# Optimization experiments

Hardware: AMD Instinct MI355X
Metric: run time of the kernel (lower is better)

## Reference

```python
import jax, jax.numpy as jnp
import numpy as np

B, L, HID, H = 4, 1024, 1024, 16
D = HID // H  # 64

def setup_inputs() -> dict:
    key = jax.random.key(0)
    ks = jax.random.split(key, 9)
    s = 0.02
    return {
        'query_states': jax.random.normal(ks[0], (B, L, HID), jnp.float32),
        'key_states':   jax.random.normal(ks[1], (B, L, HID), jnp.float32),
        'value_states': jax.random.normal(ks[2], (B, L, HID), jnp.float32),
        'Wq': jax.random.normal(ks[3], (HID, HID), jnp.float32) * s,
        'bq': jnp.zeros((HID,), jnp.float32),
        'Wk': jax.random.normal(ks[4], (HID, HID), jnp.float32) * s,
        'bk': jnp.zeros((HID,), jnp.float32),
        'Wv': jax.random.normal(ks[5], (HID, HID), jnp.float32) * s,
        'bv': jnp.zeros((HID,), jnp.float32),
        'Wo': jax.random.normal(ks[6], (HID, HID), jnp.float32) * s,
        'bo': jnp.zeros((HID,), jnp.float32),
        'rel_pos_enc': jax.random.normal(ks[7], (2 * L - 1, D), jnp.float32),
    }

def _split_heads(x):
    # [B,L,HID] -> [B,H,L,D]
    return x.reshape(B, L, H, D).transpose(0, 2, 1, 3)

def reference(query_states, key_states, value_states, Wq, bq, Wk, bk, Wv, bv, Wo, bo, rel_pos_enc):
    q = _split_heads(query_states @ Wq + bq)  # [B,H,L,D]
    k = _split_heads(key_states @ Wk + bk)
    v = _split_heads(value_states @ Wv + bv)
    scores = jnp.einsum('bhld,bhrd->bhlr', q, k)
    # relative position bias
    pos = jnp.arange(L)
    distance = pos[:, None] - pos[None, :] + L - 1          # [L,L] in [0, 2L-2]
    pos_emb = rel_pos_enc[distance]                          # [L,L,D]
    scores = scores + jnp.einsum('bhld,lrd->bhlr', q, pos_emb)
    scores = scores / jnp.sqrt(jnp.asarray(D, scores.dtype))
    probs = jax.nn.softmax(scores, axis=-1)                  # dropout p=0 (eval)
    ctx = jnp.einsum('bhlr,bhrd->bhld', probs, v)
    ctx = ctx.transpose(0, 2, 1, 3).reshape(B, L, HID)
    out = ctx @ Wo + bo
    return (out, probs)
```

## Files before the change

kernel.cpp:

```cpp
#include <hip/hip_runtime.h>

typedef __bf16 bf16_t;
typedef bf16_t bf16x8 __attribute__((ext_vector_type(8)));
typedef bf16_t bf16x4 __attribute__((ext_vector_type(4)));
typedef float f32x16 __attribute__((ext_vector_type(16)));
typedef float f32x4v __attribute__((ext_vector_type(4)));
typedef unsigned int u32;

#define DEVI __device__ __forceinline__

DEVI f32x16 zero16() {
  f32x16 z;
#pragma unroll
  for (int i = 0; i < 16; ++i) z[i] = 0.0f;
  return z;
}

DEVI void gload16(const bf16_t* g, const unsigned short* l) {
  __builtin_amdgcn_global_load_lds(
      (const __attribute__((address_space(1))) u32*)g,
      (__attribute__((address_space(3))) u32*)l, 16, 0, 0);
}

union U16B { bf16x8 v; uint4 u; unsigned short s[8]; };
union U4B  { bf16_t h[4]; uint2 u; };

__global__ __launch_bounds__(256) void prep_kernel(
    const float* __restrict__ W0, const float* __restrict__ W1,
    const float* __restrict__ W2, const float* __restrict__ W3,
    bf16_t* __restrict__ T0, bf16_t* __restrict__ T1,
    bf16_t* __restrict__ T2, bf16_t* __restrict__ T3,
    const float* __restrict__ xq, const float* __restrict__ xk,
    const float* __restrict__ xv, const float* __restrict__ relE,
    bf16_t* __restrict__ xqb, bf16_t* __restrict__ xkb,
    bf16_t* __restrict__ xvb, bf16_t* __restrict__ Eb) {
  __shared__ float T[64][65];
  const int bid = blockIdx.x;
  const int tid = threadIdx.x;
  if (bid < 1024) {
    const int sel = bid >> 8;
    const float* W = sel == 0 ? W0 : sel == 1 ? W1 : sel == 2 ? W2 : W3;
    bf16_t* Wt = sel == 0 ? T0 : sel == 1 ? T1 : sel == 2 ? T2 : T3;
    const int bx = bid & 255;
    const int tx = bx & 15, ty = bx >> 4;
    const int k0 = ty * 64, n0 = tx * 64;
    {
      const int r = tid >> 4, c4 = (tid & 15) * 4;
#pragma unroll
      for (int rr = 0; rr < 64; rr += 16) {
        float4 v = *reinterpret_cast<const float4*>(&W[(size_t)(k0 + r + rr) * 1024 + n0 + c4]);
        T[r + rr][c4 + 0] = v.x; T[r + rr][c4 + 1] = v.y;
        T[r + rr][c4 + 2] = v.z; T[r + rr][c4 + 3] = v.w;
      }
    }
    __syncthreads();
    {
      const int r = tid >> 3, c8 = (tid & 7) * 8;
#pragma unroll
      for (int rr = 0; rr < 64; rr += 32) {
        U16B p;
#pragma unroll
        for (int i = 0; i < 8; ++i) p.v[i] = (bf16_t)T[c8 + i][r + rr];
        *reinterpret_cast<uint4*>(&Wt[(size_t)(n0 + r + rr) * 1024 + k0 + c8]) = p.u;
      }
    }
  } else {
    for (int u = (bid - 1024) * 256 + tid; u < 3178496; u += 2048 * 256) {
      if (u < 3145728) {
        const int which = u >> 20;
        const float* src = which == 0 ? xq : which == 1 ? xk : xv;
        bf16_t* dst = which == 0 ? xqb : which == 1 ? xkb : xvb;
        const size_t off = (size_t)(u & 1048575) * 4;
        float4 v = *reinterpret_cast<const float4*>(&src[off]);
        U4B p;
        p.h[0] = (bf16_t)v.x; p.h[1] = (bf16_t)v.y; p.h[2] = (bf16_t)v.z; p.h[3] = (bf16_t)v.w;
        *reinterpret_cast<uint2*>(&dst[off]) = p.u;
      } else {
        const int q = u - 3145728;
        U4B p;
        if (q < 32752) {
          float4 v = *reinterpret_cast<const float4*>(&relE[(size_t)q * 4]);
          p.h[0] = (bf16_t)v.x; p.h[1] = (bf16_t)v.y; p.h[2] = (bf16_t)v.z; p.h[3] = (bf16_t)v.w;
        } else {
          p.h[0] = p.h[1] = p.h[2] = p.h[3] = (bf16_t)0.0f;
        }
        *reinterpret_cast<uint2*>(&Eb[(size_t)q * 4]) = p.u;
      }
    }
  }
}

#define ROWMAP(reg) (((reg) & 3) + 8 * ((reg) >> 2) + 4 * hi)
template <int MODE>
__global__ __launch_bounds__(256) void gemm_kernel(
    const bf16_t* __restrict__ A0, const bf16_t* __restrict__ A1,
    const bf16_t* __restrict__ A2, const bf16_t* __restrict__ W0,
    const bf16_t* __restrict__ W1, const bf16_t* __restrict__ W2,
    const float* __restrict__ b0, const float* __restrict__ b1,
    const float* __restrict__ b2, void* __restrict__ O0,
    void* __restrict__ O1, void* __restrict__ O2) {
  __shared__ __align__(16) unsigned short As[128][64];
  __shared__ __align__(16) unsigned short Bs[128][64];
  const int f = blockIdx.x;
  int op, r;
  const bf16_t *Ap, *Wt;
  const float* bias;
  void* Out;
  if constexpr (MODE == 0) {
    const int fp = (f & 7) * 96 + (f >> 3);
    op = fp >> 8; r = fp & 255;
    Ap = op == 0 ? A0 : op == 1 ? A1 : A2;
    Wt = op == 0 ? W0 : op == 1 ? W1 : W2;
    bias = op == 0 ? b0 : op == 1 ? b1 : b2;
    Out = op == 0 ? O0 : op == 1 ? O1 : O2;
  } else {
    const int fp = (f & 7) * 32 + (f >> 3);
    op = 0; r = fp;
    Ap = A0; Wt = W0; bias = b0; Out = O0;
  }
  const int m0 = (r >> 3) * 128, n0 = (r & 7) * 128;
  const int tid = threadIdx.x;
  const int lane = tid & 63, wave = tid >> 6;
  const int hi = lane >> 5, ln = lane & 31;
  const int wr = wave >> 1, wc = wave & 1;
  const int srow = lane >> 3, scol = lane & 7;

  f32x16 acc[2][2];
  acc[0][0] = zero16(); acc[0][1] = zero16();
  acc[1][0] = zero16(); acc[1][1] = zero16();

  for (int k0 = 0; k0 < 1024; k0 += 64) {
#pragma unroll
    for (int j = 0; j < 4; ++j) {
      const int rowbase = wave * 32 + j * 8;
      const int row = rowbase + srow;
      const int gc = scol ^ (row & 7);
      gload16(&Ap[(size_t)(m0 + row) * 1024 + k0 + gc * 8], &As[rowbase][0]);
      gload16(&Wt[(size_t)(n0 + row) * 1024 + k0 + gc * 8], &Bs[rowbase][0]);
    }
    __syncthreads();
#pragma unroll
    for (int kk = 0; kk < 4; ++kk) {
      const int ch = kk * 2 + hi;
      const int ar0 = wr * 64 + ln, ar1 = ar0 + 32;
      const int br0 = wc * 64 + ln, br1 = br0 + 32;
      bf16x8 a0 = *reinterpret_cast<const bf16x8*>(&As[ar0][(ch ^ (ar0 & 7)) * 8]);
      bf16x8 a1 = *reinterpret_cast<const bf16x8*>(&As[ar1][(ch ^ (ar1 & 7)) * 8]);
      bf16x8 bb0 = *reinterpret_cast<const bf16x8*>(&Bs[br0][(ch ^ (br0 & 7)) * 8]);
      bf16x8 bb1 = *reinterpret_cast<const bf16x8*>(&Bs[br1][(ch ^ (br1 & 7)) * 8]);
      acc[0][0] = __builtin_amdgcn_mfma_f32_32x32x16_bf16(a0, bb0, acc[0][0], 0, 0, 0);
      acc[0][1] = __builtin_amdgcn_mfma_f32_32x32x16_bf16(a0, bb1, acc[0][1], 0, 0, 0);
      acc[1][0] = __builtin_amdgcn_mfma_f32_32x32x16_bf16(a1, bb0, acc[1][0], 0, 0, 0);
      acc[1][1] = __builtin_amdgcn_mfma_f32_32x32x16_bf16(a1, bb1, acc[1][1], 0, 0, 0);
    }
    __syncthreads();
  }
#pragma unroll
  for (int cb = 0; cb < 2; ++cb) {
    const int nc = n0 + wc * 64 + cb * 32 + ln;
    const float bv = bias[nc];
    if constexpr (MODE == 2) {
#pragma unroll
      for (int rb = 0; rb < 2; ++rb)
#pragma unroll
        for (int reg = 0; reg < 16; ++reg) {
          const int mr = m0 + wr * 64 + rb * 32 + ROWMAP(reg);
          ((float*)Out)[(size_t)mr * 1024 + nc] = acc[rb][cb][reg] + bv;
        }
    } else {
      const int h = nc >> 6, d = nc & 63;
      if (op < 2) {
#pragma unroll
        for (int rb = 0; rb < 2; ++rb)
#pragma unroll
          for (int reg = 0; reg < 16; ++reg) {
            const int mr = m0 + wr * 64 + rb * 32 + ROWMAP(reg);
            const int b = mr >> 10, l = mr & 1023;
            ((bf16_t*)Out)[(((size_t)(b * 16 + h)) * 1024 + l) * 64 + d] =
                (bf16_t)(acc[rb][cb][reg] + bv);
          }
      } else {
#pragma unroll
        for (int rb = 0; rb < 2; ++rb)
#pragma unroll
          for (int g = 0; g < 4; ++g) {
            const int l4 = m0 + wr * 64 + rb * 32 + g * 8 + 4 * hi;
            const int b = l4 >> 10, ll = l4 & 1023;
            U4B p;
#pragma unroll
            for (int j = 0; j < 4; ++j) p.h[j] = (bf16_t)(acc[rb][cb][g * 4 + j] + bv);
            *reinterpret_cast<uint2*>(
                &((bf16_t*)Out)[(((size_t)(b * 16 + h)) * 64 + d) * 1024 + ll]) = p.u;
          }
      }
    }
  }
}

__global__ __launch_bounds__(512, 4) void attn_kernel(
    const bf16_t* __restrict__ q, const bf16_t* __restrict__ k,
    const bf16_t* __restrict__ vt, const bf16_t* __restrict__ E,
    float* __restrict__ probs, bf16_t* __restrict__ ctx) {
  __shared__ __align__(16) unsigned short Pbuf[8][32][128];
  __shared__ float rstat[32][9];
  const int f = blockIdx.x;
  const int fp = (f & 7) * 256 + (f >> 3);
  const int bh = fp >> 5;
  const int l0 = (fp & 31) * 32;
  const int tid = threadIdx.x;
  const int lane = tid & 63, wave = tid >> 6;
  const int hi = lane >> 5, ln = lane & 31;
  const bf16_t* qb = q + (size_t)bh * 1024 * 64;
  const bf16_t* kb = k + (size_t)bh * 1024 * 64;
  const bf16_t* vb = vt + (size_t)bh * 64 * 1024;
  const int rbase = wave * 128;
  const int b0 = l0 - rbase + 992;

  bf16x8 qf[4];
#pragma unroll
  for (int kk = 0; kk < 4; ++kk)
    qf[kk] = *reinterpret_cast<const bf16x8*>(&qb[(size_t)(l0 + ln) * 64 + kk * 16 + hi * 8]);

  f32x16 tpre = zero16();
  __builtin_amdgcn_s_setprio(1);
#pragma unroll
  for (int kk = 0; kk < 4; ++kk) {
    bf16x8 e = *reinterpret_cast<const bf16x8*>(
        &E[(size_t)(b0 + 32 + ln) * 64 + kk * 16 + hi * 8]);
    tpre = __builtin_amdgcn_mfma_f32_32x32x16_bf16(qf[kk], e, tpre, 0, 0, 0);
  }
  __builtin_amdgcn_s_setprio(0);

#pragma unroll
  for (int t = 0; t < 4; ++t) {
    const int r0 = rbase + t * 32;
    f32x16 acc = zero16();
    f32x16 tcur = zero16();
    __builtin_amdgcn_s_setprio(1);
#pragma unroll
    for (int kk = 0; kk < 4; ++kk) {
      bf16x8 kf = *reinterpret_cast<const bf16x8*>(
          &kb[(size_t)(r0 + ln) * 64 + kk * 16 + hi * 8]);
      acc = __builtin_amdgcn_mfma_f32_32x32x16_bf16(qf[kk], kf, acc, 0, 0, 0);
      bf16x8 e = *reinterpret_cast<const bf16x8*>(
          &E[(size_t)(b0 - 32 * t + ln) * 64 + kk * 16 + hi * 8]);
      tcur = __builtin_amdgcn_mfma_f32_32x32x16_bf16(qf[kk], e, tcur, 0, 0, 0);
    }
    __builtin_amdgcn_s_setprio(0);
#pragma unroll
    for (int reg = 0; reg < 16; ++reg) {
      const int i = ROWMAP(reg);
      const int w = i - ln + 31;
      const int src = (w & 31) + (hi << 5);
      acc[reg] += __shfl((ln >= i) ? tcur[reg] : tpre[reg], src, 64);
    }
    const int col = t * 32 + ln;
#pragma unroll
    for (int reg = 0; reg < 16; ++reg) {
      const int i = ROWMAP(reg);
      union { bf16_t h; unsigned short u; } cv;
      cv.h = (bf16_t)exp2f(acc[reg] * 0.1803368801f);
      Pbuf[wave][i][((col >> 3) ^ (i & 7)) * 8 + (col & 7)] = cv.u;
    }
    tpre = tcur;
  }

  {
    float s = 0.0f;
#pragma unroll
    for (int g = 0; g < 8; ++g) {
      const int cg = hi * 8 + g;
      bf16x8 pv = *reinterpret_cast<const bf16x8*>(
          &Pbuf[wave][ln][((cg ^ (ln & 7))) * 8]);
#pragma unroll
      for (int e = 0; e < 8; ++e) s += (float)pv[e];
    }
    s += __shfl_xor(s, 32, 64);
    if (hi == 0) rstat[ln][wave] = s;
  }

  f32x16 pv0 = zero16(), pv1 = zero16();
  __builtin_amdgcn_s_setprio(1);
#pragma unroll
  for (int kk = 0; kk < 8; ++kk) {
    const int ch = kk * 2 + hi;
    bf16x8 pa = *reinterpret_cast<const bf16x8*>(&Pbuf[wave][ln][(ch ^ (ln & 7)) * 8]);
    bf16x8 v0 = *reinterpret_cast<const bf16x8*>(
        &vb[(size_t)ln * 1024 + rbase + kk * 16 + hi * 8]);
    bf16x8 v1 = *reinterpret_cast<const bf16x8*>(
        &vb[(size_t)(32 + ln) * 1024 + rbase + kk * 16 + hi * 8]);
    pv0 = __builtin_amdgcn_mfma_f32_32x32x16_bf16(pa, v0, pv0, 0, 0, 0);
    pv1 = __builtin_amdgcn_mfma_f32_32x32x16_bf16(pa, v1, pv1, 0, 0, 0);
  }
  __builtin_amdgcn_s_setprio(0);

  __syncthreads();

  float inv;
  {
    float s = 0.0f;
#pragma unroll
    for (int w = 0; w < 8; ++w) s += rstat[ln][w];
    inv = 1.0f / s;
  }

  float* pb = probs + ((size_t)bh * 1024 + l0) * 1024;
#pragma unroll
  for (int it = 0; it < 16; ++it) {
    const int r = it * 2 + hi;
    const float invr = __shfl(inv, r, 64);
    const int g = ln >> 1;
    bf16x4 pv = *reinterpret_cast<const bf16x4*>(
        &Pbuf[wave][r][(g ^ (r & 7)) * 8 + (ln & 1) * 4]);
    f32x4v o;
    o[0] = (float)pv[0] * invr; o[1] = (float)pv[1] * invr;
    o[2] = (float)pv[2] * invr; o[3] = (float)pv[3] * invr;
    __builtin_nontemporal_store(
        o, reinterpret_cast<f32x4v*>(&pb[(size_t)r * 1024 + rbase + ln * 4]));
  }

  float* cred = reinterpret_cast<float*>(&Pbuf[0][0][0]);
  if (wave < 4) {
#pragma unroll
    for (int reg = 0; reg < 16; ++reg) {
      const int i = ROWMAP(reg);
      cred[((size_t)wave * 32 + i) * 64 + ln] = pv0[reg];
      cred[((size_t)wave * 32 + i) * 64 + 32 + ln] = pv1[reg];
    }
  }
  __syncthreads();
  if (wave >= 4) {
    const int s = wave - 4;
#pragma unroll
    for (int reg = 0; reg < 16; ++reg) {
      const int i = ROWMAP(reg);
      cred[((size_t)s * 32 + i) * 64 + ln] += pv0[reg];
      cred[((size_t)s * 32 + i) * 64 + 32 + ln] += pv1[reg];
    }
  }
  __syncthreads();
  {
    const int i = tid >> 4, d0 = (tid & 15) * 4;
    float4 a = *reinterpret_cast<const float4*>(&cred[(size_t)(0 * 32 + i) * 64 + d0]);
#pragma unroll
    for (int s = 1; s < 4; ++s) {
      float4 b = *reinterpret_cast<const float4*>(&cred[(size_t)(s * 32 + i) * 64 + d0]);
      a.x += b.x; a.y += b.y; a.z += b.z; a.w += b.w;
    }
    const float invr = __shfl(inv, i, 64);
    U4B o;
    o.h[0] = (bf16_t)(a.x * invr); o.h[1] = (bf16_t)(a.y * invr);
    o.h[2] = (bf16_t)(a.z * invr); o.h[3] = (bf16_t)(a.w * invr);
    const int b = bh >> 4, h = bh & 15;
    *reinterpret_cast<uint2*>(&ctx[((((size_t)b * 1024) + l0 + i) * 16 + h) * 64 + d0]) = o.u;
  }
}

extern "C" void kernel_launch(void* const* d_in, const int* in_sizes, int n_in,
                              void* d_out, int out_size, void* d_ws, size_t ws_size,
                              hipStream_t stream) {
  const float* xq = (const float*)d_in[0];
  const float* xk = (const float*)d_in[1];
  const float* xv = (const float*)d_in[2];
  const float* Wq = (const float*)d_in[3];
  const float* bq = (const float*)d_in[4];
  const float* Wk = (const float*)d_in[5];
  const float* bk = (const float*)d_in[6];
  const float* Wv = (const float*)d_in[7];
  const float* bv = (const float*)d_in[8];
  const float* Wo = (const float*)d_in[9];
  const float* bo = (const float*)d_in[10];
  const float* relE = (const float*)d_in[11];

  char* ws = (char*)d_ws;
  const size_t MB2 = 1u << 21;
  bf16_t* WtQ = (bf16_t*)(ws + 0 * MB2);
  bf16_t* WtK = (bf16_t*)(ws + 1 * MB2);
  bf16_t* WtV = (bf16_t*)(ws + 2 * MB2);
  bf16_t* WtO = (bf16_t*)(ws + 3 * MB2);
  bf16_t* Eb  = (bf16_t*)(ws + 4 * MB2);
  bf16_t* qb  = (bf16_t*)(ws + 4 * MB2 + (1u << 19));
  bf16_t* kb  = qb + (size_t)4 * 16 * 1024 * 64;
  bf16_t* vtb = kb + (size_t)4 * 16 * 1024 * 64;
  bf16_t* ctxb = vtb + (size_t)4 * 16 * 1024 * 64;

  float* outp = (float*)d_out;
  float* probs = outp + (size_t)4 * 1024 * 1024;
  bf16_t* xqb = (bf16_t*)probs;
  bf16_t* xkb = xqb + (size_t)4 * 1024 * 1024;
  bf16_t* xvb = xkb + (size_t)4 * 1024 * 1024;

  prep_kernel<<<3072, 256, 0, stream>>>(Wq, Wk, Wv, Wo, WtQ, WtK, WtV, WtO,
                                        xq, xk, xv, relE, xqb, xkb, xvb, Eb);
  gemm_kernel<0><<<768, 256, 0, stream>>>(xqb, xkb, xvb, WtQ, WtK, WtV,
                                          bq, bk, bv, qb, kb, vtb);
  attn_kernel<<<2048, 512, 0, stream>>>(qb, kb, vtb, Eb, probs, ctxb);
  gemm_kernel<2><<<256, 256, 0, stream>>>(ctxb, nullptr, nullptr, WtO, nullptr, nullptr,
                                          bo, nullptr, nullptr, outp, nullptr, nullptr);
}
```

Baseline: 200.3 us.

## Compute softmax row sums via MFMA, widen probs stores, simplify ctx reduction

Row sums of the exponentiated scores are now produced by an extra MFMA against a vector of ones inside the PV loop, replacing the separate LDS read-and-add pass. exp2f is replaced by the hardware exp2 builtin. The probs write-out now uses 8-element LDS reads and two 16-byte stores per lane. The two-stage cross-wave ctx reduction is replaced by every wave writing its partial into its own Pbuf slice, followed by one 8-way sum, which removes a barrier. The costs are an extra MFMA per step and a sum taken from bf16 values at MFMA precision, with a different rounding order.

```diff
diff --git a/kernel.cpp b/kernel.cpp
--- a/kernel.cpp
+++ b/kernel.cpp
@@ -14,6 +14,14 @@
 #pragma unroll
   for (int i = 0; i < 16; ++i) z[i] = 0.0f;
   return z;
+}
+
+DEVI float fast_exp2(float x) {
+#if __has_builtin(__builtin_amdgcn_exp2f)
+  return __builtin_amdgcn_exp2f(x);
+#else
+  return exp2f(x);
+#endif
 }
 
 DEVI void gload16(const bf16_t* g, const unsigned short* l) {
@@ -259,27 +267,16 @@
     for (int reg = 0; reg < 16; ++reg) {
       const int i = ROWMAP(reg);
       union { bf16_t h; unsigned short u; } cv;
-      cv.h = (bf16_t)exp2f(acc[reg] * 0.1803368801f);
+      cv.h = (bf16_t)fast_exp2(acc[reg] * 0.1803368801f);
       Pbuf[wave][i][((col >> 3) ^ (i & 7)) * 8 + (col & 7)] = cv.u;
     }
     tpre = tcur;
   }
 
-  {
-    float s = 0.0f;
-#pragma unroll
-    for (int g = 0; g < 8; ++g) {
-      const int cg = hi * 8 + g;
-      bf16x8 pv = *reinterpret_cast<const bf16x8*>(
-          &Pbuf[wave][ln][((cg ^ (ln & 7))) * 8]);
-#pragma unroll
-      for (int e = 0; e < 8; ++e) s += (float)pv[e];
-    }
-    s += __shfl_xor(s, 32, 64);
-    if (hi == 0) rstat[ln][wave] = s;
-  }
-
-  f32x16 pv0 = zero16(), pv1 = zero16();
+  bf16x8 ones;
+#pragma unroll
+  for (int e = 0; e < 8; ++e) ones[e] = (bf16_t)1.0f;
+  f32x16 pv0 = zero16(), pv1 = zero16(), pvs = zero16();
   __builtin_amdgcn_s_setprio(1);
 #pragma unroll
   for (int kk = 0; kk < 8; ++kk) {
@@ -291,9 +288,16 @@
         &vb[(size_t)(32 + ln) * 1024 + rbase + kk * 16 + hi * 8]);
     pv0 = __builtin_amdgcn_mfma_f32_32x32x16_bf16(pa, v0, pv0, 0, 0, 0);
     pv1 = __builtin_amdgcn_mfma_f32_32x32x16_bf16(pa, v1, pv1, 0, 0, 0);
+    pvs = __builtin_amdgcn_mfma_f32_32x32x16_bf16(pa, ones, pvs, 0, 0, 0);
   }
   __builtin_amdgcn_s_setprio(0);
 
+  {
+    float s = 0.0f;
+#pragma unroll
+    for (int reg = 0; reg < 16; ++reg) s = ((ln & 15) == reg) ? pvs[reg] : s;
+    if (ln < 16) rstat[ROWMAP(ln)][wave] = s;
+  }
   __syncthreads();
 
   float inv;
@@ -305,46 +309,42 @@
   }
 
   float* pb = probs + ((size_t)bh * 1024 + l0) * 1024;
-#pragma unroll
-  for (int it = 0; it < 16; ++it) {
-    const int r = it * 2 + hi;
-    const float invr = __shfl(inv, r, 64);
-    const int g = ln >> 1;
-    bf16x4 pv = *reinterpret_cast<const bf16x4*>(
-        &Pbuf[wave][r][(g ^ (r & 7)) * 8 + (ln & 1) * 4]);
-    f32x4v o;
-    o[0] = (float)pv[0] * invr; o[1] = (float)pv[1] * invr;
-    o[2] = (float)pv[2] * invr; o[3] = (float)pv[3] * invr;
-    __builtin_nontemporal_store(
-        o, reinterpret_cast<f32x4v*>(&pb[(size_t)r * 1024 + rbase + ln * 4]));
-  }
-
-  float* cred = reinterpret_cast<float*>(&Pbuf[0][0][0]);
-  if (wave < 4) {
-#pragma unroll
-    for (int reg = 0; reg < 16; ++reg) {
-      const int i = ROWMAP(reg);
-      cred[((size_t)wave * 32 + i) * 64 + ln] = pv0[reg];
-      cred[((size_t)wave * 32 + i) * 64 + 32 + ln] = pv1[reg];
-    }
-  }
-  __syncthreads();
-  if (wave >= 4) {
-    const int s = wave - 4;
-#pragma unroll
-    for (int reg = 0; reg < 16; ++reg) {
-      const int i = ROWMAP(reg);
-      cred[((size_t)s * 32 + i) * 64 + ln] += pv0[reg];
-      cred[((size_t)s * 32 + i) * 64 + 32 + ln] += pv1[reg];
-    }
+  {
+    const int rsub = lane >> 4;
+    const int pg = lane & 15;
+#pragma unroll
+    for (int it = 0; it < 8; ++it) {
+      const int r = it * 4 + rsub;
+      const float invr = __shfl(inv, r, 64);
+      bf16x8 pv = *reinterpret_cast<const bf16x8*>(
+          &Pbuf[wave][r][(pg ^ (r & 7)) * 8]);
+      f32x4v o0, o1;
+      o0[0] = (float)pv[0] * invr; o0[1] = (float)pv[1] * invr;
+      o0[2] = (float)pv[2] * invr; o0[3] = (float)pv[3] * invr;
+      o1[0] = (float)pv[4] * invr; o1[1] = (float)pv[5] * invr;
+      o1[2] = (float)pv[6] * invr; o1[3] = (float)pv[7] * invr;
+      float* dst = &pb[(size_t)r * 1024 + rbase + pg * 8];
+      __builtin_nontemporal_store(o0, reinterpret_cast<f32x4v*>(dst));
+      __builtin_nontemporal_store(o1, reinterpret_cast<f32x4v*>(dst + 4));
+    }
+  }
+
+  float* credw = reinterpret_cast<float*>(&Pbuf[wave][0][0]);
+#pragma unroll
+  for (int reg = 0; reg < 16; ++reg) {
+    const int i = ROWMAP(reg);
+    credw[(size_t)i * 64 + ln] = pv0[reg];
+    credw[(size_t)i * 64 + 32 + ln] = pv1[reg];
   }
   __syncthreads();
   {
     const int i = tid >> 4, d0 = (tid & 15) * 4;
-    float4 a = *reinterpret_cast<const float4*>(&cred[(size_t)(0 * 32 + i) * 64 + d0]);
-#pragma unroll
-    for (int s = 1; s < 4; ++s) {
-      float4 b = *reinterpret_cast<const float4*>(&cred[(size_t)(s * 32 + i) * 64 + d0]);
+    const float* cred = reinterpret_cast<const float*>(&Pbuf[0][0][0]);
+    float4 a = *reinterpret_cast<const float4*>(&cred[(size_t)i * 64 + d0]);
+#pragma unroll
+    for (int s = 1; s < 8; ++s) {
+      float4 b = *reinterpret_cast<const float4*>(
+          &cred[(size_t)s * 2048 + (size_t)i * 64 + d0]);
       a.x += b.x; a.y += b.y; a.z += b.z; a.w += b.w;
     }
     const float invr = __shfl(inv, i, 64);
```

Result: slower. 237.5 us (+18.6%).

## Use 256x256 double-buffered tiles for the fused QKV projection GEMM

Applied to the files above, without the earlier changes.

Splits the templated GEMM into a dedicated QKV kernel and an output-projection kernel. The QKV kernel now uses 512-thread blocks over 256x256 tiles with two LDS buffers, prefetching the next K-tile via async global-to-LDS loads while computing on the current one (vmcnt-based waits instead of full syncs). This targets load latency and operand reuse at the cost of larger LDS use (128KB per block), fewer blocks (192 on a machine with many CUs), and more register pressure.

```diff
diff --git a/kernel.cpp b/kernel.cpp
--- a/kernel.cpp
+++ b/kernel.cpp
@@ -91,33 +91,128 @@
 }
 
 #define ROWMAP(reg) (((reg) & 3) + 8 * ((reg) >> 2) + 4 * hi)
-template <int MODE>
-__global__ __launch_bounds__(256) void gemm_kernel(
+
+__global__ __launch_bounds__(512, 2) void gemm_qkv_kernel(
     const bf16_t* __restrict__ A0, const bf16_t* __restrict__ A1,
     const bf16_t* __restrict__ A2, const bf16_t* __restrict__ W0,
     const bf16_t* __restrict__ W1, const bf16_t* __restrict__ W2,
     const float* __restrict__ b0, const float* __restrict__ b1,
-    const float* __restrict__ b2, void* __restrict__ O0,
-    void* __restrict__ O1, void* __restrict__ O2) {
+    const float* __restrict__ b2, bf16_t* __restrict__ O0,
+    bf16_t* __restrict__ O1, bf16_t* __restrict__ O2) {
+  __shared__ __align__(16) unsigned short As[2][256][64];
+  __shared__ __align__(16) unsigned short Bs[2][256][64];
+  const int f = blockIdx.x;
+  const int fp = (f & 7) * 24 + (f >> 3);
+  const int op = fp >> 6;
+  const int r = fp & 63;
+  const bf16_t* Ap = op == 0 ? A0 : op == 1 ? A1 : A2;
+  const bf16_t* Wt = op == 0 ? W0 : op == 1 ? W1 : W2;
+  const float* bias = op == 0 ? b0 : op == 1 ? b1 : b2;
+  bf16_t* Out = op == 0 ? O0 : op == 1 ? O1 : O2;
+  const int m0 = (r >> 2) * 256, n0 = (r & 3) * 256;
+  const int tid = threadIdx.x;
+  const int lane = tid & 63, wave = tid >> 6;
+  const int hi = lane >> 5, ln = lane & 31;
+  const int wr = wave >> 2, wc = wave & 3;
+  const int srow = lane >> 3, scol = lane & 7;
+
+  f32x16 acc[4][2];
+#pragma unroll
+  for (int rt = 0; rt < 4; ++rt) { acc[rt][0] = zero16(); acc[rt][1] = zero16(); }
+
+#define STAGE(kt, buf)                                                              \
+  {                                                                                 \
+    _Pragma("unroll")                                                               \
+    for (int j = 0; j < 4; ++j) {                                                   \
+      const int rowbase = wave * 32 + j * 8;                                        \
+      const int row = rowbase + srow;                                               \
+      const int gc = scol ^ (row & 7);                                              \
+      gload16(&Ap[(size_t)(m0 + row) * 1024 + (kt) * 64 + gc * 8],                  \
+              &As[buf][rowbase][0]);                                                \
+      gload16(&Wt[(size_t)(n0 + row) * 1024 + (kt) * 64 + gc * 8],                  \
+              &Bs[buf][rowbase][0]);                                                \
+    }                                                                               \
+  }
+
+  STAGE(0, 0);
+  STAGE(1, 1);
+
+  for (int kt = 0; kt < 16; ++kt) {
+    const int cur = kt & 1;
+    if (kt < 15) {
+      asm volatile("s_waitcnt vmcnt(8)" ::: "memory");
+    } else {
+      asm volatile("s_waitcnt vmcnt(0)" ::: "memory");
+    }
+    __builtin_amdgcn_s_barrier();
+    __builtin_amdgcn_sched_barrier(0);
+#pragma unroll
+    for (int kk = 0; kk < 4; ++kk) {
+      const int ch = kk * 2 + hi;
+      bf16x8 a[4], b[2];
+#pragma unroll
+      for (int rt = 0; rt < 4; ++rt) {
+        const int ar = wr * 128 + rt * 32 + ln;
+        a[rt] = *reinterpret_cast<const bf16x8*>(&As[cur][ar][(ch ^ (ar & 7)) * 8]);
+      }
+#pragma unroll
+      for (int ct = 0; ct < 2; ++ct) {
+        const int br = wc * 64 + ct * 32 + ln;
+        b[ct] = *reinterpret_cast<const bf16x8*>(&Bs[cur][br][(ch ^ (br & 7)) * 8]);
+      }
+#pragma unroll
+      for (int rt = 0; rt < 4; ++rt)
+#pragma unroll
+        for (int ct = 0; ct < 2; ++ct)
+          acc[rt][ct] = __builtin_amdgcn_mfma_f32_32x32x16_bf16(a[rt], b[ct], acc[rt][ct], 0, 0, 0);
+    }
+    __builtin_amdgcn_sched_barrier(0);
+    __builtin_amdgcn_s_barrier();
+    __builtin_amdgcn_sched_barrier(0);
+    if (kt + 2 < 16) STAGE(kt + 2, cur);
+  }
+#undef STAGE
+
+#pragma unroll
+  for (int ct = 0; ct < 2; ++ct) {
+    const int nc = n0 + wc * 64 + ct * 32 + ln;
+    const float bv = bias[nc];
+    const int h = nc >> 6, d = nc & 63;
+    if (op < 2) {
+#pragma unroll
+      for (int rt = 0; rt < 4; ++rt)
+#pragma unroll
+        for (int reg = 0; reg < 16; ++reg) {
+          const int mr = m0 + wr * 128 + rt * 32 + ROWMAP(reg);
+          const int b = mr >> 10, l = mr & 1023;
+          Out[(((size_t)(b * 16 + h)) * 1024 + l) * 64 + d] =
+              (bf16_t)(acc[rt][ct][reg] + bv);
+        }
+    } else {
+#pragma unroll
+      for (int rt = 0; rt < 4; ++rt)
+#pragma unroll
+        for (int g = 0; g < 4; ++g) {
+          const int l4 = m0 + wr * 128 + rt * 32 + g * 8 + 4 * hi;
+          const int b = l4 >> 10, ll = l4 & 1023;
+          U4B p;
+#pragma unroll
+          for (int j = 0; j < 4; ++j) p.h[j] = (bf16_t)(acc[rt][ct][g * 4 + j] + bv);
+          *reinterpret_cast<uint2*>(
+              &Out[(((size_t)(b * 16 + h)) * 64 + d) * 1024 + ll]) = p.u;
+        }
+    }
+  }
+}
+
+__global__ __launch_bounds__(256) void gemm_o_kernel(
+    const bf16_t* __restrict__ A0, const bf16_t* __restrict__ W0,
+    const float* __restrict__ b0, float* __restrict__ O0) {
   __shared__ __align__(16) unsigned short As[128][64];
   __shared__ __align__(16) unsigned short Bs[128][64];
   const int f = blockIdx.x;
-  int op, r;
-  const bf16_t *Ap, *Wt;
-  const float* bias;
-  void* Out;
-  if constexpr (MODE == 0) {
-    const int fp = (f & 7) * 96 + (f >> 3);
-    op = fp >> 8; r = fp & 255;
-    Ap = op == 0 ? A0 : op == 1 ? A1 : A2;
-    Wt = op == 0 ? W0 : op == 1 ? W1 : W2;
-    bias = op == 0 ? b0 : op == 1 ? b1 : b2;
-    Out = op == 0 ? O0 : op == 1 ? O1 : O2;
-  } else {
-    const int fp = (f & 7) * 32 + (f >> 3);
-    op = 0; r = fp;
-    Ap = A0; Wt = W0; bias = b0; Out = O0;
-  }
+  const int fp = (f & 7) * 32 + (f >> 3);
+  const int r = fp;
   const int m0 = (r >> 3) * 128, n0 = (r & 7) * 128;
   const int tid = threadIdx.x;
   const int lane = tid & 63, wave = tid >> 6;
@@ -135,8 +230,8 @@
       const int rowbase = wave * 32 + j * 8;
       const int row = rowbase + srow;
       const int gc = scol ^ (row & 7);
-      gload16(&Ap[(size_t)(m0 + row) * 1024 + k0 + gc * 8], &As[rowbase][0]);
-      gload16(&Wt[(size_t)(n0 + row) * 1024 + k0 + gc * 8], &Bs[rowbase][0]);
+      gload16(&A0[(size_t)(m0 + row) * 1024 + k0 + gc * 8], &As[rowbase][0]);
+      gload16(&W0[(size_t)(n0 + row) * 1024 + k0 + gc * 8], &Bs[rowbase][0]);
     }
     __syncthreads();
 #pragma unroll
@@ -158,42 +253,14 @@
 #pragma unroll
   for (int cb = 0; cb < 2; ++cb) {
     const int nc = n0 + wc * 64 + cb * 32 + ln;
-    const float bv = bias[nc];
-    if constexpr (MODE == 2) {
-#pragma unroll
-      for (int rb = 0; rb < 2; ++rb)
-#pragma unroll
-        for (int reg = 0; reg < 16; ++reg) {
-          const int mr = m0 + wr * 64 + rb * 32 + ROWMAP(reg);
-          ((float*)Out)[(size_t)mr * 1024 + nc] = acc[rb][cb][reg] + bv;
-        }
-    } else {
-      const int h = nc >> 6, d = nc & 63;
-      if (op < 2) {
-#pragma unroll
-        for (int rb = 0; rb < 2; ++rb)
-#pragma unroll
-          for (int reg = 0; reg < 16; ++reg) {
-            const int mr = m0 + wr * 64 + rb * 32 + ROWMAP(reg);
-            const int b = mr >> 10, l = mr & 1023;
-            ((bf16_t*)Out)[(((size_t)(b * 16 + h)) * 1024 + l) * 64 + d] =
-                (bf16_t)(acc[rb][cb][reg] + bv);
-          }
-      } else {
-#pragma unroll
-        for (int rb = 0; rb < 2; ++rb)
-#pragma unroll
-          for (int g = 0; g < 4; ++g) {
-            const int l4 = m0 + wr * 64 + rb * 32 + g * 8 + 4 * hi;
-            const int b = l4 >> 10, ll = l4 & 1023;
-            U4B p;
-#pragma unroll
-            for (int j = 0; j < 4; ++j) p.h[j] = (bf16_t)(acc[rb][cb][g * 4 + j] + bv);
-            *reinterpret_cast<uint2*>(
-                &((bf16_t*)Out)[(((size_t)(b * 16 + h)) * 64 + d) * 1024 + ll]) = p.u;
-          }
-      }
-    }
+    const float bv = b0[nc];
+#pragma unroll
+    for (int rb = 0; rb < 2; ++rb)
+#pragma unroll
+      for (int reg = 0; reg < 16; ++reg) {
+        const int mr = m0 + wr * 64 + rb * 32 + ROWMAP(reg);
+        O0[(size_t)mr * 1024 + nc] = acc[rb][cb][reg] + bv;
+      }
   }
 }
 
@@ -392,9 +459,8 @@
 
   prep_kernel<<<3072, 256, 0, stream>>>(Wq, Wk, Wv, Wo, WtQ, WtK, WtV, WtO,
                                         xq, xk, xv, relE, xqb, xkb, xvb, Eb);
-  gemm_kernel<0><<<768, 256, 0, stream>>>(xqb, xkb, xvb, WtQ, WtK, WtV,
-                                          bq, bk, bv, qb, kb, vtb);
+  gemm_qkv_kernel<<<192, 512, 0, stream>>>(xqb, xkb, xvb, WtQ, WtK, WtV,
+                                           bq, bk, bv, qb, kb, vtb);
   attn_kernel<<<2048, 512, 0, stream>>>(qb, kb, vtb, Eb, probs, ctxb);
-  gemm_kernel<2><<<256, 256, 0, stream>>>(ctxb, nullptr, nullptr, WtO, nullptr, nullptr,
-                                          bo, nullptr, nullptr, outp, nullptr, nullptr);
-}
+  gemm_o_kernel<<<256, 256, 0, stream>>>(ctxb, WtO, bo, outp);
+}
```

After: 196.8 us. No clear change (-1.7%).
